# Performance work log

Hardware: AMD Instinct MI355X
Metric: run time of the kernel (lower is better)

Reference implementation:

```python
import jax, jax.numpy as jnp
import numpy as np

DIM = 1024
HEADS = 16
D_HEAD = 64
INNER = HEADS * D_HEAD  # 1024
CTX_DIM = 768
FF_INNER = 4 * DIM  # 4096
EPS = 1e-5
SCALE = D_HEAD ** -0.5


def _layer_norm(x, g, b):
    m = jnp.mean(x, axis=-1, keepdims=True)
    v = jnp.mean(jnp.square(x - m), axis=-1, keepdims=True)
    return (x - m) * jax.lax.rsqrt(v + EPS) * g + b


def _attention(x, ctx, wq, wk, wv, wo, bo):
    B, S, _ = x.shape
    T = ctx.shape[1]
    # project and split heads -> [B, H, S, Dh]
    q = (x @ wq).reshape(B, S, HEADS, D_HEAD).transpose(0, 2, 1, 3)
    k = (ctx @ wk).reshape(B, T, HEADS, D_HEAD).transpose(0, 2, 1, 3)
    v = (ctx @ wv).reshape(B, T, HEADS, D_HEAD).transpose(0, 2, 1, 3)
    attn = jnp.einsum('bhid,bhjd->bhij', q, k) * SCALE
    attn = jax.nn.softmax(attn, axis=-1)
    out = jnp.einsum('bhij,bhjd->bhid', attn, v)  # [B, H, S, Dh]
    out = out.transpose(0, 2, 1, 3).reshape(B, S, INNER)
    return out @ wo + bo


def setup_inputs() -> dict:
    key = jax.random.key(0)
    ks = jax.random.split(key, 20)
    rn = lambda k, shape, s=0.02: jax.random.normal(k, shape, dtype=jnp.float32) * s
    inp = {
        'hidden_states': jax.random.normal(ks[0], (4, 2048, DIM), dtype=jnp.float32),
        'context': jax.random.normal(ks[1], (4, 77, CTX_DIM), dtype=jnp.float32),
        # self-attention
        'wq1': rn(ks[2], (DIM, INNER)), 'wk1': rn(ks[3], (DIM, INNER)),
        'wv1': rn(ks[4], (DIM, INNER)),
        'wo1': rn(ks[5], (INNER, DIM)), 'bo1': jnp.zeros((DIM,), jnp.float32),
        # cross-attention (k/v from context dim 768)
        'wq2': rn(ks[6], (DIM, INNER)), 'wk2': rn(ks[7], (CTX_DIM, INNER)),
        'wv2': rn(ks[8], (CTX_DIM, INNER)),
        'wo2': rn(ks[9], (INNER, DIM)), 'bo2': jnp.zeros((DIM,), jnp.float32),
        # GEGLU feed-forward
        'w_ff1': rn(ks[10], (DIM, 2 * FF_INNER)), 'b_ff1': jnp.zeros((2 * FF_INNER,), jnp.float32),
        'w_ff2': rn(ks[11], (FF_INNER, DIM)), 'b_ff2': jnp.zeros((DIM,), jnp.float32),
        # layer norms
        'ln1_g': jnp.ones((DIM,), jnp.float32), 'ln1_b': jnp.zeros((DIM,), jnp.float32),
        'ln2_g': jnp.ones((DIM,), jnp.float32), 'ln2_b': jnp.zeros((DIM,), jnp.float32),
        'ln3_g': jnp.ones((DIM,), jnp.float32), 'ln3_b': jnp.zeros((DIM,), jnp.float32),
    }
    return inp


def reference(hidden_states, context, wq1, wk1, wv1, wo1, bo1,
              wq2, wk2, wv2, wo2, bo2, w_ff1, b_ff1, w_ff2, b_ff2,
              ln1_g, ln1_b, ln2_g, ln2_b, ln3_g, ln3_b):
    # self-attention, pre-norm residual
    h = hidden_states
    h = h + _attention(_layer_norm(h, ln1_g, ln1_b), _layer_norm(h, ln1_g, ln1_b),
                       wq1, wk1, wv1, wo1, bo1)
    # cross-attention
    h = h + _attention(_layer_norm(h, ln2_g, ln2_b), context,
                       wq2, wk2, wv2, wo2, bo2)
    # GEGLU feed-forward
    x = _layer_norm(h, ln3_g, ln3_b) @ w_ff1 + b_ff1
    lin, gate = jnp.split(x, 2, axis=2)
    h = h + (lin * jax.nn.gelu(gate)) @ w_ff2 + b_ff2
    return h
```

## Files before the change

### kernel.cpp

```cpp
#include <hip/hip_runtime.h>

#define DIMM 1024
#define NHEADS 16
#define DHEAD 64
#define BATCH 4
#define SEQ 2048
#define TCTX 77
#define CTXD 768
#define FFI 4096

typedef float f32x4 __attribute__((ext_vector_type(4)));
typedef __bf16 bf16x8 __attribute__((ext_vector_type(8)));

__device__ __forceinline__ float bf2f(unsigned short u){
  union { unsigned int i; float f; } c; c.i = ((unsigned int)u) << 16; return c.f;
}
__device__ __forceinline__ unsigned short f2bf(float f){
  union { float f; unsigned int i; } c; c.f = f;
  unsigned int i = c.i;
  return (unsigned short)((i + 0x7fffu + ((i >> 16) & 1u)) >> 16);
}
__device__ __forceinline__ void cp16(const unsigned short* g, unsigned short* l){
  __builtin_amdgcn_global_load_lds(
      (const __attribute__((address_space(1))) unsigned int*)g,
      (__attribute__((address_space(3))) unsigned int*)l, 16, 0, 0);
}

__global__ __launch_bounds__(256) void ln_kernel(const float* __restrict__ x,
                                                 const float* __restrict__ g,
                                                 const float* __restrict__ bb,
                                                 unsigned short* __restrict__ y)
{
  int row = blockIdx.x, tid = threadIdx.x;
  float4 raw = ((const float4*)(x + (size_t)row * DIMM))[tid];
  float v0 = raw.x, v1 = raw.y, v2 = raw.z, v3 = raw.w;
  float s  = v0 + v1 + v2 + v3;
  float sq = v0*v0 + v1*v1 + v2*v2 + v3*v3;
  #pragma unroll
  for (int off = 32; off; off >>= 1){ s += __shfl_xor(s, off); sq += __shfl_xor(sq, off); }
  __shared__ float sm[8];
  int wave = tid >> 6, lane = tid & 63;
  if (lane == 0){ sm[wave] = s; sm[4 + wave] = sq; }
  __syncthreads();
  s  = sm[0] + sm[1] + sm[2] + sm[3];
  sq = sm[4] + sm[5] + sm[6] + sm[7];
  float mean = s * (1.f / DIMM);
  float var  = sq * (1.f / DIMM) - mean * mean;
  float rstd = rsqrtf(var + 1e-5f);
  float4 gr = ((const float4*)g)[tid];
  float4 br = ((const float4*)bb)[tid];
  ushort4 o;
  o.x = f2bf((v0 - mean) * rstd * gr.x + br.x);
  o.y = f2bf((v1 - mean) * rstd * gr.y + br.y);
  o.z = f2bf((v2 - mean) * rstd * gr.z + br.z);
  o.w = f2bf((v3 - mean) * rstd * gr.w + br.w);
  ((ushort4*)(y + (size_t)row * DIMM))[tid] = o;
}

__global__ __launch_bounds__(256) void wt_kernel(const float* __restrict__ in,
                                                 unsigned short* __restrict__ out,
                                                 int K, int N)
{
  __shared__ float t[32][33];
  int tx = threadIdx.x & 31, ty = threadIdx.x >> 5;
  int k0 = blockIdx.y * 32, n0 = blockIdx.x * 32;
  #pragma unroll
  for (int i = 0; i < 4; i++)
    t[ty + i * 8][tx] = in[(size_t)(k0 + ty + i * 8) * N + n0 + tx];
  __syncthreads();
  #pragma unroll
  for (int i = 0; i < 4; i++)
    out[(size_t)(n0 + ty + i * 8) * K + k0 + tx] = f2bf(t[tx][ty + i * 8]);
}

#define CTXE (TCTX * BATCH * CTXD)
__global__ __launch_bounds__(256) void ctxcvt_kernel(const float* __restrict__ in,
                                                     unsigned short* __restrict__ out)
{
  int e = (blockIdx.x * 256 + threadIdx.x) * 4;
  float4 v;
  if (e < CTXE) v = *(const float4*)(in + e);
  else { v.x = 0.f; v.y = 0.f; v.z = 0.f; v.w = 0.f; }
  ushort4 o; o.x = f2bf(v.x); o.y = f2bf(v.y); o.z = f2bf(v.z); o.w = f2bf(v.w);
  *(ushort4*)(out + e) = o;
}

template<int RESF, int CF32>
__global__ __launch_bounds__(256) void gemm_bt(
    const unsigned short* __restrict__ A, int lda,
    const unsigned short* __restrict__ Bt, int ldb,
    const float* __restrict__ bias, const void* __restrict__ resv,
    void* __restrict__ Cv, int ldc,
    int M, int N, int K)
{
  __shared__ __align__(16) unsigned short As[128][64];
  __shared__ __align__(16) unsigned short Bs[128][64];
  int tid = threadIdx.x;
  int n0 = blockIdx.x * 128, row0 = blockIdx.y * 128;
  int wave = tid >> 6, lane = tid & 63, quad = lane >> 4, l16 = lane & 15;
  int wm = (wave >> 1) * 64, wn = (wave & 1) * 64;
  int wrow = wave * 32;
  int lrow = lane >> 3, lgrp = lane & 7;
  int gcol = ((lgrp ^ lrow) * 8);

  f32x4 acc[4][4];
  #pragma unroll
  for (int mt = 0; mt < 4; mt++)
    #pragma unroll
    for (int nt = 0; nt < 4; nt++) acc[mt][nt] = 0.f;

  for (int k0 = 0; k0 < K; k0 += 64) {
    const unsigned short* ga = A  + (size_t)(row0 + wrow + lrow) * lda + k0 + gcol;
    const unsigned short* gb = Bt + (size_t)(n0  + wrow + lrow) * ldb + k0 + gcol;
    #pragma unroll
    for (int i = 0; i < 4; i++){
      cp16(ga + (size_t)(8 * i) * lda, &As[wrow + 8 * i][0]);
      cp16(gb + (size_t)(8 * i) * ldb, &Bs[wrow + 8 * i][0]);
    }
    __syncthreads();
    #pragma unroll
    for (int kc = 0; kc < 2; kc++){
      bf16x8 af[4], bf[4];
      #pragma unroll
      for (int mt = 0; mt < 4; mt++){
        int R = wm + mt * 16 + l16;
        af[mt] = *(const bf16x8*)&As[R][((kc * 4 + quad) ^ (R & 7)) * 8];
      }
      #pragma unroll
      for (int nt = 0; nt < 4; nt++){
        int R = wn + nt * 16 + l16;
        bf[nt] = *(const bf16x8*)&Bs[R][((kc * 4 + quad) ^ (R & 7)) * 8];
      }
      #pragma unroll
      for (int mt = 0; mt < 4; mt++)
        #pragma unroll
        for (int nt = 0; nt < 4; nt++)
          acc[mt][nt] = __builtin_amdgcn_mfma_f32_16x16x32_bf16(af[mt], bf[nt], acc[mt][nt], 0, 0, 0);
    }
    __syncthreads();
  }

  #pragma unroll
  for (int nt = 0; nt < 4; nt++){
    int c = n0 + wn + nt * 16 + l16;
    float bv = bias ? bias[c] : 0.f;
    #pragma unroll
    for (int mt = 0; mt < 4; mt++){
      int rbase = row0 + wm + mt * 16 + quad * 4;
      #pragma unroll
      for (int rr = 0; rr < 4; rr++){
        int r = rbase + rr;
        if (r < M) {
          float val = acc[mt][nt][rr] + bv;
          size_t idx = (size_t)r * ldc + c;
          if (RESF) val += ((const float*)resv)[idx];
          if (CF32) ((float*)Cv)[idx] = val;
          else      ((unsigned short*)Cv)[idx] = f2bf(val);
        }
      }
    }
  }
}

__global__ __launch_bounds__(512, 4) void ff1_geglu_bt(
    const unsigned short* __restrict__ A,
    const unsigned short* __restrict__ BtW,
    const float* __restrict__ bias,
    unsigned short* __restrict__ Z, int M)
{
  __shared__ __align__(16) unsigned short As[128][64];
  __shared__ __align__(16) unsigned short BsL[128][64];
  __shared__ __align__(16) unsigned short BsG[128][64];
  int tid = threadIdx.x;
  int n0 = blockIdx.x * 128, row0 = blockIdx.y * 128;
  int wave = tid >> 6, lane = tid & 63, quad = lane >> 4, l16 = lane & 15;
  int wm = (wave >> 2) * 64, wn = (wave & 3) * 32;
  int wrow = wave * 16;
  int lrow = lane >> 3, lgrp = lane & 7;
  int gcol = ((lgrp ^ lrow) * 8);

  f32x4 accL[4][2], accG[4][2];
  #pragma unroll
  for (int mt = 0; mt < 4; mt++)
    #pragma unroll
    for (int nt = 0; nt < 2; nt++){ accL[mt][nt] = 0.f; accG[mt][nt] = 0.f; }

  for (int k0 = 0; k0 < DIMM; k0 += 64) {
    const unsigned short* ga = A   + (size_t)(row0 + wrow + lrow) * DIMM + k0 + gcol;
    const unsigned short* gl = BtW + (size_t)(n0  + wrow + lrow) * DIMM + k0 + gcol;
    const unsigned short* gg = BtW + (size_t)(FFI + n0 + wrow + lrow) * DIMM + k0 + gcol;
    #pragma unroll
    for (int i = 0; i < 2; i++){
      cp16(ga + (size_t)(8 * i) * DIMM, &As[wrow + 8 * i][0]);
      cp16(gl + (size_t)(8 * i) * DIMM, &BsL[wrow + 8 * i][0]);
      cp16(gg + (size_t)(8 * i) * DIMM, &BsG[wrow + 8 * i][0]);
    }
    __syncthreads();
    #pragma unroll
    for (int kc = 0; kc < 2; kc++){
      bf16x8 af[4], bl[2], bg[2];
      #pragma unroll
      for (int mt = 0; mt < 4; mt++){
        int R = wm + mt * 16 + l16;
        af[mt] = *(const bf16x8*)&As[R][((kc * 4 + quad) ^ (R & 7)) * 8];
      }
      #pragma unroll
      for (int nt = 0; nt < 2; nt++){
        int R = wn + nt * 16 + l16;
        bl[nt] = *(const bf16x8*)&BsL[R][((kc * 4 + quad) ^ (R & 7)) * 8];
        bg[nt] = *(const bf16x8*)&BsG[R][((kc * 4 + quad) ^ (R & 7)) * 8];
      }
      #pragma unroll
      for (int mt = 0; mt < 4; mt++)
        #pragma unroll
        for (int nt = 0; nt < 2; nt++){
          accL[mt][nt] = __builtin_amdgcn_mfma_f32_16x16x32_bf16(af[mt], bl[nt], accL[mt][nt], 0, 0, 0);
          accG[mt][nt] = __builtin_amdgcn_mfma_f32_16x16x32_bf16(af[mt], bg[nt], accG[mt][nt], 0, 0, 0);
        }
    }
    __syncthreads();
  }

  #pragma unroll
  for (int nt = 0; nt < 2; nt++){
    int c = n0 + wn + nt * 16 + l16;
    float bvL = bias[c];
    float bvG = bias[c + FFI];
    #pragma unroll
    for (int mt = 0; mt < 4; mt++){
      int rbase = row0 + wm + mt * 16 + quad * 4;
      #pragma unroll
      for (int rr = 0; rr < 4; rr++){
        float lin = accL[mt][nt][rr] + bvL;
        float g   = accG[mt][nt][rr] + bvG;
        float y = 0.7978845608028654f * (g + 0.044715f * g * g * g);
        float e = __builtin_amdgcn_exp2f(y * 2.8853900817779268f);
        float t = 1.f - 2.f * __builtin_amdgcn_rcpf(e + 1.f);
        Z[(size_t)(rbase + rr) * FFI + c] = f2bf(lin * 0.5f * g * (1.f + t));
      }
    }
  }
}

__global__ __launch_bounds__(512, 4) void attn_mfma(
    const unsigned short* __restrict__ Q, int ldq,
    const unsigned short* __restrict__ Kb,
    const unsigned short* __restrict__ Vb, int ldkv,
    unsigned short* __restrict__ O,
    int S, int T, float scale)
{
  int tid = threadIdx.x, wave = tid >> 6, lane = tid & 63;
  int quad = lane >> 4, l16 = lane & 15;
  int bh = blockIdx.y, b = bh >> 4, h = bh & 15;
  int qw = blockIdx.x * 256 + wave * 32;

  __shared__ __align__(16) unsigned short Ks[64][64];
  __shared__ __align__(16) unsigned short Vp[64][64];

  float qs = scale * 1.44269504088896f;
  bf16x8 Qf[2][2];
  #pragma unroll
  for (int mt = 0; mt < 2; mt++)
    #pragma unroll
    for (int kc = 0; kc < 2; kc++){
      const unsigned short* qp = Q + ((size_t)b * S + qw + mt * 16 + l16) * ldq
                                   + h * DHEAD + kc * 32 + quad * 8;
      union { float4 v; unsigned short u[8]; } ld; ld.v = *(const float4*)qp;
      union { bf16x8 v; unsigned short u[8]; } sc;
      #pragma unroll
      for (int j = 0; j < 8; j++) sc.u[j] = f2bf(bf2f(ld.u[j]) * qs);
      Qf[mt][kc] = sc.v;
    }

  f32x4 Oacc[2][4];
  float lp[2] = {0.f, 0.f};
  #pragma unroll
  for (int mt = 0; mt < 2; mt++)
    #pragma unroll
    for (int nt = 0; nt < 4; nt++) Oacc[mt][nt] = 0.f;

  int lrow = lane >> 3, lgrp = lane & 7;
  int gcol = (lgrp ^ lrow) * 8;
  int vj = lane;
  int vchunk = ((vj >> 5) << 2) | ((vj >> 2) & 3);
  int velem  = (((vj >> 4) & 1) << 2) | (vj & 3);
  int dbs = wave * 8;

  for (int j0 = 0; j0 < T; j0 += 64){
    bool tail = (j0 + 64 > T);
    if (!tail){
      const unsigned short* gk = Kb + ((size_t)b * T + j0 + wave * 8 + lrow) * ldkv
                                    + h * DHEAD + gcol;
      cp16(gk, &Ks[wave * 8][0]);
    } else {
      int key = tid >> 3, g = tid & 7;
      float4 kv;
      if (j0 + key < T) kv = *(const float4*)(Kb + ((size_t)b * T + j0 + key) * ldkv + h * DHEAD + g * 8);
      else { kv.x = 0.f; kv.y = 0.f; kv.z = 0.f; kv.w = 0.f; }
      *(float4*)&Ks[key][(g ^ (key & 7)) * 8] = kv;
    }
    {
      union { float4 v; unsigned short u[8]; } vv;
      if (j0 + vj < T) vv.v = *(const float4*)(Vb + ((size_t)b * T + j0 + vj) * ldkv + h * DHEAD + dbs);
      else { vv.v.x = 0.f; vv.v.y = 0.f; vv.v.z = 0.f; vv.v.w = 0.f; }
      #pragma unroll
      for (int u = 0; u < 8; u++)
        Vp[dbs + u][((vchunk ^ u) << 3) | velem] = vv.u[u];
    }
    __syncthreads();

    union pfu { bf16x8 v; __bf16 e[8]; } pf[2][2];
    #pragma unroll
    for (int mt = 0; mt < 2; mt++){
      f32x4 sT[4];
      #pragma unroll
      for (int nt = 0; nt < 4; nt++){
        sT[nt] = 0.f;
        #pragma unroll
        for (int kc = 0; kc < 2; kc++){
          bf16x8 kf = *(const bf16x8*)&Ks[nt * 16 + l16][((kc * 4 + quad) ^ (l16 & 7)) * 8];
          sT[nt] = __builtin_amdgcn_mfma_f32_16x16x32_bf16(kf, Qf[mt][kc], sT[nt], 0, 0, 0);
        }
      }
      #pragma unroll
      for (int nt = 0; nt < 4; nt++)
        #pragma unroll
        for (int rr = 0; rr < 4; rr++){
          float sv = sT[nt][rr];
          if (tail && (j0 + nt * 16 + quad * 4 + rr) >= T) sv = -1e30f;
          float p = __builtin_amdgcn_exp2f(fminf(sv, 108.f));
          lp[mt] += p;
          pf[mt][nt >> 1].e[(nt & 1) * 4 + rr] = (__bf16)p;
        }
    }

    #pragma unroll
    for (int kc = 0; kc < 2; kc++)
      #pragma unroll
      for (int nt = 0; nt < 4; nt++){
        int R = nt * 16 + l16;
        bf16x8 vf = *(const bf16x8*)&Vp[R][((kc * 4 + quad) ^ (R & 7)) * 8];
        #pragma unroll
        for (int mt = 0; mt < 2; mt++)
          Oacc[mt][nt] = __builtin_amdgcn_mfma_f32_16x16x32_bf16(pf[mt][kc].v, vf, Oacc[mt][nt], 0, 0, 0);
      }
    __syncthreads();
  }

  #pragma unroll
  for (int mt = 0; mt < 2; mt++){
    float l = lp[mt];
    l += __shfl_xor(l, 16);
    l += __shfl_xor(l, 32);
    float inv[4];
    #pragma unroll
    for (int rr = 0; rr < 4; rr++)
      inv[rr] = 1.f / __shfl(l, quad * 4 + rr);
    #pragma unroll
    for (int nt = 0; nt < 4; nt++)
      #pragma unroll
      for (int rr = 0; rr < 4; rr++){
        size_t idx = ((size_t)b * S + qw + mt * 16 + quad * 4 + rr) * DIMM
                     + h * DHEAD + nt * 16 + l16;
        O[idx] = f2bf(Oacc[mt][nt][rr] * inv[rr]);
      }
  }
}

extern "C" void kernel_launch(void* const* d_in, const int* in_sizes, int n_in,
                              void* d_out, int out_size, void* d_ws, size_t ws_size,
                              hipStream_t stream)
{
  const float* h0   = (const float*)d_in[0];
  const float* ctx  = (const float*)d_in[1];
  const float* wq1  = (const float*)d_in[2];
  const float* wk1  = (const float*)d_in[3];
  const float* wv1  = (const float*)d_in[4];
  const float* wo1  = (const float*)d_in[5];
  const float* bo1  = (const float*)d_in[6];
  const float* wq2  = (const float*)d_in[7];
  const float* wk2  = (const float*)d_in[8];
  const float* wv2  = (const float*)d_in[9];
  const float* wo2  = (const float*)d_in[10];
  const float* bo2  = (const float*)d_in[11];
  const float* wff1 = (const float*)d_in[12];
  const float* bff1 = (const float*)d_in[13];
  const float* wff2 = (const float*)d_in[14];
  const float* bff2 = (const float*)d_in[15];
  const float* ln1g = (const float*)d_in[16];
  const float* ln1b = (const float*)d_in[17];
  const float* ln2g = (const float*)d_in[18];
  const float* ln2b = (const float*)d_in[19];
  const float* ln3g = (const float*)d_in[20];
  const float* ln3b = (const float*)d_in[21];

  unsigned short* wsp = (unsigned short*)d_ws;
  const size_t RD = (size_t)BATCH * SEQ * DIMM;
  unsigned short* xn  = wsp;
  unsigned short* qkv = wsp + RD;
  unsigned short* ar  = wsp + 4 * RD;
  unsigned short* zb  = qkv;
  float* hres = (float*)d_out;

  const size_t M1 = (size_t)1024 * 1024;
  const int ROWS = BATCH * SEQ;
  const int CROWS = BATCH * TCTX;
  const float scale = 0.125f;
  dim3 blk(256);
  dim3 ablk(512);
  dim3 attn_grid(SEQ / 256, BATCH * NHEADS);

  wt_kernel<<<dim3(32, 32), blk, 0, stream>>>(wq1, ar,          DIMM, DIMM);
  wt_kernel<<<dim3(32, 32), blk, 0, stream>>>(wk1, ar + M1,     DIMM, DIMM);
  wt_kernel<<<dim3(32, 32), blk, 0, stream>>>(wv1, ar + 2 * M1, DIMM, DIMM);
  wt_kernel<<<dim3(32, 32), blk, 0, stream>>>(wo1, ar + 3 * M1, DIMM, DIMM);
  ln_kernel<<<ROWS, blk, 0, stream>>>(h0, ln1g, ln1b, xn);
  gemm_bt<0,0><<<dim3(3072 / 128, ROWS / 128), blk, 0, stream>>>(
      xn, DIMM, ar, DIMM, nullptr, nullptr, qkv, 3072, ROWS, 3072, DIMM);
  attn_mfma<<<attn_grid, ablk, 0, stream>>>(qkv, 3072, qkv + 1024, qkv + 2048, 3072, xn, SEQ, SEQ, scale);
  gemm_bt<1,1><<<dim3(DIMM / 128, ROWS / 128), blk, 0, stream>>>(
      xn, DIMM, ar + 3 * M1, DIMM, bo1, h0, hres, DIMM, ROWS, DIMM, DIMM);

  unsigned short* wq2T  = ar;
  unsigned short* wkv2T = ar + M1;
  unsigned short* wo2T  = ar + M1 + (size_t)2048 * CTXD;
  unsigned short* xc    = wo2T + M1;
  wt_kernel<<<dim3(32, 32), blk, 0, stream>>>(wq2, wq2T, DIMM, DIMM);
  wt_kernel<<<dim3(32, 24), blk, 0, stream>>>(wk2, wkv2T, CTXD, DIMM);
  wt_kernel<<<dim3(32, 24), blk, 0, stream>>>(wv2, wkv2T + (size_t)1024 * CTXD, CTXD, DIMM);
  wt_kernel<<<dim3(32, 32), blk, 0, stream>>>(wo2, wo2T, DIMM, DIMM);
  ctxcvt_kernel<<<(384 * CTXD / 4) / 256, blk, 0, stream>>>(ctx, xc);
  ln_kernel<<<ROWS, blk, 0, stream>>>(hres, ln2g, ln2b, xn);
  gemm_bt<0,0><<<dim3(DIMM / 128, ROWS / 128), blk, 0, stream>>>(
      xn, DIMM, wq2T, DIMM, nullptr, nullptr, qkv, DIMM, ROWS, DIMM, DIMM);
  unsigned short* kvc = qkv + RD;
  gemm_bt<0,0><<<dim3(2048 / 128, 3), blk, 0, stream>>>(
      xc, CTXD, wkv2T, CTXD, nullptr, nullptr, kvc, 2048, CROWS, 2048, CTXD);
  attn_mfma<<<attn_grid, ablk, 0, stream>>>(qkv, 1024, kvc, kvc + 1024, 2048, xn, SEQ, TCTX, scale);
  gemm_bt<1,1><<<dim3(DIMM / 128, ROWS / 128), blk, 0, stream>>>(
      xn, DIMM, wo2T, DIMM, bo2, hres, hres, DIMM, ROWS, DIMM, DIMM);

  unsigned short* wff1T = ar;
  unsigned short* wff2T = ar + 8 * M1;
  wt_kernel<<<dim3(256, 32),  blk, 0, stream>>>(wff1, wff1T, DIMM, 2 * FFI);
  wt_kernel<<<dim3(32, 128),  blk, 0, stream>>>(wff2, wff2T, FFI, DIMM);
  ln_kernel<<<ROWS, blk, 0, stream>>>(hres, ln3g, ln3b, xn);
  for (int half = 0; half < 2; half++){
    int r0 = half * 4096;
    ff1_geglu_bt<<<dim3(FFI / 128, 4096 / 128), dim3(512), 0, stream>>>(
        xn + (size_t)r0 * DIMM, wff1T, bff1, zb, 4096);
    gemm_bt<1,1><<<dim3(DIMM / 128, 4096 / 128), blk, 0, stream>>>(
        zb, FFI, wff2T, FFI, bff2, hres + (size_t)r0 * DIMM,
        hres + (size_t)r0 * DIMM, DIMM, 4096, DIMM, FFI);
  }
}
```

Measured before the change: 921.1 us.

## Double-buffer K/V tiles in attention kernel to overlap loads with MFMA

The attention kernel now keeps two LDS buffers for the K and V tiles. It prefetches the next 64-key tile, with K going asynchronously to LDS and V into registers, while computing on the current tile. This leaves one barrier per iteration instead of two, so global load latency can hide behind the QK and PV MFMAs. The cost is double the LDS footprint and extra live registers for the V prefetch. With T=77 there are only two tiles, so the overlap available is limited, and the kernel is only one part of the total time.

```diff
diff --git a/kernel.cpp b/kernel.cpp
--- a/kernel.cpp
+++ b/kernel.cpp
@@ -254,8 +254,8 @@
   int bh = blockIdx.y, b = bh >> 4, h = bh & 15;
   int qw = blockIdx.x * 256 + wave * 32;
 
-  __shared__ __align__(16) unsigned short Ks[64][64];
-  __shared__ __align__(16) unsigned short Vp[64][64];
+  __shared__ __align__(16) unsigned short Ks[2][64][64];
+  __shared__ __align__(16) unsigned short Vp[2][64][64];
 
   float qs = scale * 1.44269504088896f;
   bf16x8 Qf[2][2];
@@ -286,29 +286,52 @@
   int velem  = (((vj >> 4) & 1) << 2) | (vj & 3);
   int dbs = wave * 8;
 
+  const unsigned short* Kbase = Kb + (size_t)b * T * ldkv + h * DHEAD;
+  const unsigned short* Vbase = Vb + (size_t)b * T * ldkv + h * DHEAD;
+
+  union vregs { float4 v; unsigned short u[8]; };
+
+  #define STAGE_K(j0_, bi_) do {                                              \
+    if ((j0_) + 64 <= T){                                                     \
+      const unsigned short* gk = Kbase + (size_t)((j0_) + wave * 8 + lrow) * ldkv + gcol; \
+      cp16(gk, &Ks[bi_][wave * 8][0]);                                        \
+    } else {                                                                  \
+      int key_ = tid >> 3, g_ = tid & 7;                                      \
+      float4 kv_;                                                             \
+      if ((j0_) + key_ < T) kv_ = *(const float4*)(Kbase + (size_t)((j0_) + key_) * ldkv + g_ * 8); \
+      else { kv_.x = 0.f; kv_.y = 0.f; kv_.z = 0.f; kv_.w = 0.f; }            \
+      *(float4*)&Ks[bi_][key_][(g_ ^ (key_ & 7)) * 8] = kv_;                  \
+    } } while(0)
+
+  #define LOAD_V(j0_, dst_) do {                                              \
+    if ((j0_) + vj < T) dst_.v = *(const float4*)(Vbase + (size_t)((j0_) + vj) * ldkv + dbs); \
+    else { dst_.v.x = 0.f; dst_.v.y = 0.f; dst_.v.z = 0.f; dst_.v.w = 0.f; }  \
+    } while(0)
+
+  #define SCATTER_V(bi_, src_) do {                                           \
+    _Pragma("unroll")                                                         \
+    for (int u_ = 0; u_ < 8; u_++)                                            \
+      Vp[bi_][dbs + u_][((vchunk ^ u_) << 3) | velem] = src_.u[u_];           \
+    } while(0)
+
+  {
+    vregs v0;
+    STAGE_K(0, 0);
+    LOAD_V(0, v0);
+    SCATTER_V(0, v0);
+  }
+  __syncthreads();
+
+  int buf = 0;
   for (int j0 = 0; j0 < T; j0 += 64){
+    bool haveNext = (j0 + 64 < T);
+    vregs vnext;
+    if (haveNext){
+      STAGE_K(j0 + 64, buf ^ 1);
+      LOAD_V(j0 + 64, vnext);
+    }
+
     bool tail = (j0 + 64 > T);
-    if (!tail){
-      const unsigned short* gk = Kb + ((size_t)b * T + j0 + wave * 8 + lrow) * ldkv
-                                    + h * DHEAD + gcol;
-      cp16(gk, &Ks[wave * 8][0]);
-    } else {
-      int key = tid >> 3, g = tid & 7;
-      float4 kv;
-      if (j0 + key < T) kv = *(const float4*)(Kb + ((size_t)b * T + j0 + key) * ldkv + h * DHEAD + g * 8);
-      else { kv.x = 0.f; kv.y = 0.f; kv.z = 0.f; kv.w = 0.f; }
-      *(float4*)&Ks[key][(g ^ (key & 7)) * 8] = kv;
-    }
-    {
-      union { float4 v; unsigned short u[8]; } vv;
-      if (j0 + vj < T) vv.v = *(const float4*)(Vb + ((size_t)b * T + j0 + vj) * ldkv + h * DHEAD + dbs);
-      else { vv.v.x = 0.f; vv.v.y = 0.f; vv.v.z = 0.f; vv.v.w = 0.f; }
-      #pragma unroll
-      for (int u = 0; u < 8; u++)
-        Vp[dbs + u][((vchunk ^ u) << 3) | velem] = vv.u[u];
-    }
-    __syncthreads();
-
     union pfu { bf16x8 v; __bf16 e[8]; } pf[2][2];
     #pragma unroll
     for (int mt = 0; mt < 2; mt++){
@@ -318,7 +341,7 @@
         sT[nt] = 0.f;
         #pragma unroll
         for (int kc = 0; kc < 2; kc++){
-          bf16x8 kf = *(const bf16x8*)&Ks[nt * 16 + l16][((kc * 4 + quad) ^ (l16 & 7)) * 8];
+          bf16x8 kf = *(const bf16x8*)&Ks[buf][nt * 16 + l16][((kc * 4 + quad) ^ (l16 & 7)) * 8];
           sT[nt] = __builtin_amdgcn_mfma_f32_16x16x32_bf16(kf, Qf[mt][kc], sT[nt], 0, 0, 0);
         }
       }
@@ -339,13 +362,19 @@
       #pragma unroll
       for (int nt = 0; nt < 4; nt++){
         int R = nt * 16 + l16;
-        bf16x8 vf = *(const bf16x8*)&Vp[R][((kc * 4 + quad) ^ (R & 7)) * 8];
+        bf16x8 vf = *(const bf16x8*)&Vp[buf][R][((kc * 4 + quad) ^ (R & 7)) * 8];
         #pragma unroll
         for (int mt = 0; mt < 2; mt++)
           Oacc[mt][nt] = __builtin_amdgcn_mfma_f32_16x16x32_bf16(pf[mt][kc].v, vf, Oacc[mt][nt], 0, 0, 0);
       }
+
+    if (haveNext) SCATTER_V(buf ^ 1, vnext);
     __syncthreads();
-  }
+    buf ^= 1;
+  }
+  #undef STAGE_K
+  #undef LOAD_V
+  #undef SCATTER_V
 
   #pragma unroll
   for (int mt = 0; mt < 2; mt++){
```

After: 957.9 us. 4.0% more time.
